# Performance work log

Hardware: AMD Instinct MI355X
Metric: run time of the kernel (lower is better)

Reference implementation:

```python
import jax, jax.numpy as jnp
import numpy as np

EPS = 1e-5

def _ln(t, g, b):
    m = t.mean(-1, keepdims=True)
    v = ((t - m) ** 2).mean(-1, keepdims=True)
    return (t - m) * jax.lax.rsqrt(v + EPS) * g + b

def _sr(t, w, b, H, W, sr):
    # t: [B, H*W, C] -> spatial-reduction conv -> [B, (H//sr)*(W//sr), C]
    B, L, C = t.shape
    xi = t.transpose(0, 2, 1).reshape(B, C, H, W)
    y = jax.lax.conv_general_dilated(xi, w, (sr, sr), 'VALID',
                                     dimension_numbers=('NCHW', 'OIHW', 'NCHW'))
    return y.reshape(B, C, -1).transpose(0, 2, 1) + b

def setup_inputs() -> dict:
    key = jax.random.key(0)
    ks = jax.random.split(key, 9)
    C, head, sr, H, W = 128, 2, 2, 64, 64
    B, N = 4, 2 * H * W
    s = 0.02
    return {
        'x': jax.random.normal(ks[0], (B, N, C), jnp.float32),
        'qW': jax.random.normal(ks[1], (C, C), jnp.float32) * s,
        'qb': jnp.zeros((C,), jnp.float32),
        'kvW': jax.random.normal(ks[2], (C, 2 * C), jnp.float32) * s,
        'kvb': jnp.zeros((2 * C,), jnp.float32),
        'projW': jax.random.normal(ks[3], (C, C), jnp.float32) * s,
        'projb': jnp.zeros((C,), jnp.float32),
        'srW': jax.random.normal(ks[4], (C, C, sr, sr), jnp.float32) * s,
        'srb': jnp.zeros((C,), jnp.float32),
        'lnW': jnp.ones((C,), jnp.float32),
        'lnB': jnp.zeros((C,), jnp.float32),
        'H': H, 'W': W, 'fuse': 1,
    }

def reference(x, qW, qb, kvW, kvb, projW, projb, srW, srb, lnW, lnB, H, W, fuse):
    head, sr = 2, 2
    B, N, C = x.shape
    Dh = C // head
    scale = Dh ** -0.5
    q = (x @ qW + qb).reshape(B, N, head, Dh).transpose(0, 2, 1, 3)  # [B,h,N,Dh]
    mask = None
    if fuse and sr > 1:
        half = N // 2
        x_rgb = _ln(_sr(x[:, :half, :], srW, srb, H, W, sr), lnW, lnB)
        x_dte = _ln(_sr(x[:, half:, :], srW, srb, H, W, sr), lnW, lnB)
        xkv = jnp.concatenate([x_rgb, x_dte], axis=1)
        M = N // (sr * sr)
        row = jnp.arange(N)[:, None] < half            # query in rgb half
        col = jnp.arange(M)[None, :] < (M // 2)        # key in rgb half
        mask = row == col                              # True on same-modality blocks -> masked
    elif sr > 1:
        xkv = _ln(_sr(x, srW, srb, H, W, sr), lnW, lnB)
    else:
        xkv = x
    M = xkv.shape[1]
    kv = (xkv @ kvW + kvb).reshape(B, M, 2, head, Dh).transpose(2, 0, 3, 1, 4)
    k, v = kv[0], kv[1]                                # [B,h,M,Dh]
    attn = jnp.einsum('bhnd,bhmd->bhnm', q, k) * scale
    if mask is not None:
        attn = jnp.where(mask[None, None], -jnp.inf, attn)
    attn = jax.nn.softmax(attn, axis=-1)
    out = jnp.einsum('bhnm,bhmd->bhnd', attn, v).transpose(0, 2, 1, 3).reshape(B, N, C)
    return out @ projW + projb
```

## Files before the change

### kernel.cpp

```cpp
#include <hip/hip_runtime.h>
#include <hip/hip_bf16.h>

#define LN_EPS 1e-5f

typedef __attribute__((ext_vector_type(8))) short bf16x8_t;
typedef __attribute__((ext_vector_type(4))) short bf16x4_t;
typedef __attribute__((ext_vector_type(4))) float f32x4_t;
typedef __attribute__((ext_vector_type(4))) unsigned short u16x4_t;

#define MFMA32(a, b, c) __builtin_amdgcn_mfma_f32_16x16x32_bf16(a, b, c, 0, 0, 0)
#define MFMA16(a, b, c) __builtin_amdgcn_mfma_f32_16x16x16bf16_1k(a, b, c, 0, 0, 0)

__device__ inline float fast_exp2(float x) {
#if __has_builtin(__builtin_amdgcn_exp2f)
    return __builtin_amdgcn_exp2f(x);
#else
    float r;
    asm volatile("v_exp_f32 %0, %1\n\ts_nop 0" : "=v"(r) : "v"(x));
    return r;
#endif
}

__device__ inline unsigned short f2bf(float f) {
    union { float f; unsigned int u; } v; v.f = f;
    unsigned int r = v.u + 0x7fffu + ((v.u >> 16) & 1u);
    return (unsigned short)(r >> 16);
}

__device__ inline u16x4_t pk4(float a, float b, float c, float d) {
    union { u16x4_t v; __hip_bfloat162 h[2]; } u;
    u.h[0] = __float22bfloat162_rn(float2{a, b});
    u.h[1] = __float22bfloat162_rn(float2{c, d});
    return u.v;
}
__device__ inline bf16x4_t pk4b(float a, float b, float c, float d) {
    union { bf16x4_t v; __hip_bfloat162 h[2]; } u;
    u.h[0] = __float22bfloat162_rn(float2{a, b});
    u.h[1] = __float22bfloat162_rn(float2{c, d});
    return u.v;
}
__device__ inline bf16x8_t pk8(float4 a, float4 b) {
    union { bf16x8_t v; __hip_bfloat162 h[4]; } u;
    u.h[0] = __float22bfloat162_rn(float2{a.x, a.y});
    u.h[1] = __float22bfloat162_rn(float2{a.z, a.w});
    u.h[2] = __float22bfloat162_rn(float2{b.x, b.y});
    u.h[3] = __float22bfloat162_rn(float2{b.z, b.w});
    return u.v;
}

__device__ inline size_t fragidx(int row, int k, int KC) {
    return ((size_t)((row >> 4) * KC + (k >> 5))) * 512 +
           (((k >> 3) & 3) * 16 + (row & 15)) * 8 + (k & 7);
}

__global__ void k_prep_w(const float* __restrict__ qW, const float* __restrict__ kvW,
                         const float* __restrict__ projW, const float* __restrict__ srW,
                         unsigned short* __restrict__ qWs, unsigned short* __restrict__ kvWs,
                         unsigned short* __restrict__ projWs, unsigned short* __restrict__ srWs) {
    int i = blockIdx.x * 256 + threadIdx.x;
    if (i < 16384) {
        int n = i & 127, k = i >> 7;
        qWs[fragidx(n, k, 4)] = f2bf(qW[k * 128 + n]);
    } else if (i < 49152) {
        int j = i - 16384; int n = j & 255, k = j >> 8;
        kvWs[fragidx(n, k, 4)] = f2bf(kvW[k * 256 + n]);
    } else if (i < 65536) {
        int j = i - 49152; int n = j & 127, k = j >> 7;
        projWs[fragidx(n, k, 4)] = f2bf(projW[k * 128 + n]);
    } else {
        int j = i - 65536; int n = j >> 9, rem = j & 511, q = rem >> 7, c = rem & 127;
        srWs[fragidx(n, q * 128 + c, 16)] = f2bf(srW[n * 512 + c * 4 + q]);
    }
}

#define XPAD 132
__global__ __launch_bounds__(256)
void k_convkv(const float* __restrict__ x, const unsigned short* __restrict__ srWs,
              const float* __restrict__ srb, const float* __restrict__ lnW,
              const float* __restrict__ lnB, const unsigned short* __restrict__ kvWs,
              const float* __restrict__ kvb, unsigned short* __restrict__ ksw,
              unsigned short* __restrict__ vls) {
    const int t = threadIdx.x, w = t >> 6, lane = t & 63;
    const int col = lane & 15, quad = lane >> 4;
    const int RT = blockIdx.x;

    __shared__ unsigned short xl[64 * XPAD];
    __shared__ unsigned short xs[4 * 512];
    __shared__ float lnred[4][16][2];

    const int pb = RT >> 7, phf = (RT >> 6) & 1;
    const int oy = (RT >> 1) & 31, ox0 = (RT & 1) * 16;
    const int n0 = phf * 4096 + 2 * oy * 64 + 2 * ox0;
    #pragma unroll
    for (int it = 0; it < 8; it++) {
        int idx = it * 256 + t;
        int chunk = idx >> 10;
        int rr = (idx >> 5) & 31;
        int c4 = idx & 31;
        float4 v = *(const float4*)(x + ((size_t)(pb * 8192 + n0 + chunk * 64 + rr)) * 128 + c4 * 4);
        *(u16x4_t*)(xl + (chunk * 32 + rr) * XPAD + c4 * 4) = pk4(v.x, v.y, v.z, v.w);
    }
    __syncthreads();

    f32x4_t acc[2] = {};
    {
        const unsigned short* wp = srWs + lane * 8;
        #pragma unroll
        for (int kc = 0; kc < 16; kc++) {
            const int q = kc >> 2, cg = kc & 3;
            const int r = (q >> 1) * 32 + 2 * col + (q & 1);
            bf16x8_t xb = *(const bf16x8_t*)(xl + r * XPAD + cg * 32 + quad * 8);
            #pragma unroll
            for (int jj = 0; jj < 2; jj++) {
                bf16x8_t wf = *(const bf16x8_t*)(wp + (size_t)((w * 2 + jj) * 16 + kc) * 512);
                acc[jj] = MFMA32(wf, xb, acc[jj]);
            }
        }
    }
    float s = 0.f, ss = 0.f;
    #pragma unroll
    for (int jj = 0; jj < 2; jj++) {
        float4 bs = *(const float4*)(srb + (w * 2 + jj) * 16 + quad * 4);
        acc[jj][0] += bs.x; acc[jj][1] += bs.y; acc[jj][2] += bs.z; acc[jj][3] += bs.w;
        #pragma unroll
        for (int r = 0; r < 4; r++) { float v = acc[jj][r]; s += v; ss += v * v; }
    }
    s += __shfl_xor(s, 16, 64);  s += __shfl_xor(s, 32, 64);
    ss += __shfl_xor(ss, 16, 64); ss += __shfl_xor(ss, 32, 64);
    if (lane < 16) { lnred[w][lane][0] = s; lnred[w][lane][1] = ss; }
    __syncthreads();
    float stot = 0.f, sstot = 0.f;
    #pragma unroll
    for (int ww = 0; ww < 4; ww++) { stot += lnred[ww][col][0]; sstot += lnred[ww][col][1]; }
    float mean = stot * (1.0f / 128.0f);
    float var = sstot * (1.0f / 128.0f) - mean * mean;
    float rs = rsqrtf(var + LN_EPS);
    #pragma unroll
    for (int jj = 0; jj < 2; jj++) {
        int f0 = (w * 2 + jj) * 16 + quad * 4;
        float4 g = *(const float4*)(lnW + f0);
        float4 be = *(const float4*)(lnB + f0);
        u16x4_t o = pk4((acc[jj][0] - mean) * rs * g.x + be.x,
                        (acc[jj][1] - mean) * rs * g.y + be.y,
                        (acc[jj][2] - mean) * rs * g.z + be.z,
                        (acc[jj][3] - mean) * rs * g.w + be.w);
        *(u16x4_t*)(xs + ((size_t)(f0 >> 5)) * 512 +
                    (((f0 >> 3) & 3) * 16 + col) * 8 + (f0 & 7)) = o;
    }
    __syncthreads();
    bf16x8_t xf[4];
    #pragma unroll
    for (int kc = 0; kc < 4; kc++)
        xf[kc] = *(const bf16x8_t*)(xs + (size_t)kc * 512 + lane * 8);
    const int p0 = RT * 16;
    const int bb = p0 >> 11;
    #pragma unroll
    for (int jj = 0; jj < 2; jj++) {
        const int nt = w * 2 + jj;
        f32x4_t aK = {};
        #pragma unroll
        for (int kc = 0; kc < 4; kc++) {
            bf16x8_t wf = *(const bf16x8_t*)(kvWs + (size_t)(nt * 4 + kc) * 512 + lane * 8);
            aK = MFMA32(wf, xf[kc], aK);
        }
        float4 bs = *(const float4*)(kvb + nt * 16 + quad * 4);
        int m = (p0 + col) & 2047;
        int bh = bb * 2 + (nt >> 2);
        int d0 = (nt & 3) * 16 + quad * 4;
        u16x4_t o = pk4(aK[0] + bs.x, aK[1] + bs.y, aK[2] + bs.z, aK[3] + bs.w);
        *(u16x4_t*)(ksw + ((size_t)(bh * 128 + (m >> 4)) * 2 + (d0 >> 5)) * 512 +
                    (((d0 >> 3) & 3) * 16 + (m & 15)) * 8 + (d0 & 7)) = o;
    }
    #pragma unroll
    for (int jj = 0; jj < 2; jj++) {
        const int nt = w * 2 + jj;
        f32x4_t aV = {};
        #pragma unroll
        for (int kc = 0; kc < 4; kc++) {
            bf16x8_t wf = *(const bf16x8_t*)(kvWs + (size_t)((8 + nt) * 4 + kc) * 512 + lane * 8);
            aV = MFMA32(xf[kc], wf, aV);
        }
        int fv = nt * 16 + col;
        int h = fv >> 6, dd = fv & 63;
        float bv = kvb[128 + fv];
        int m0 = (p0 + quad * 4) & 2047;
        int bh = bb * 2 + h;
        int kt = m0 >> 6, nb = (m0 >> 4) & 3;
        u16x4_t o = pk4(aV[0] + bv, aV[1] + bv, aV[2] + bv, aV[3] + bv);
        *(u16x4_t*)(vls + (((size_t)(bh * 32 + kt) * 4 + (dd >> 4)) * 2 + (nb >> 1)) * 512 +
                    (quad * 16 + (dd & 15)) * 8 + (nb & 1) * 4) = o;
    }
}

__global__ __launch_bounds__(256, 2)
void k_attn_f6(const float* __restrict__ x, const unsigned short* __restrict__ qWs,
               const float* __restrict__ qb, const unsigned short* __restrict__ ksw,
               const unsigned short* __restrict__ vls, const unsigned short* __restrict__ projWs,
               const float* __restrict__ projb, float* __restrict__ out) {
    const int blkx = blockIdx.x, mod = blockIdx.y, b = blockIdx.z;
    const int t = threadIdx.x, w = t >> 6, lane = t & 63;
    const int col = lane & 15, quad = lane >> 4;
    const int qg = w & 1, h = w >> 1;
    const int bh = b * 2 + h;
    const int qbase = mod * 4096 + blkx * 64 + qg * 32;

    __shared__ unsigned short sbuf[64 * 136];

    unsigned short* qarea = sbuf + w * 2048;
    const float sc = 0.125f * 1.44269504089f;
    #pragma unroll
    for (int qt = 0; qt < 2; qt++) {
        const float* xrow = x + ((size_t)b * 8192 + qbase + qt * 16 + col) * 128;
        f32x4_t acc[4] = {};
        #pragma unroll
        for (int kc = 0; kc < 4; kc++) {
            float4 xa = *(const float4*)(xrow + kc * 32 + quad * 8);
            float4 xb2 = *(const float4*)(xrow + kc * 32 + quad * 8 + 4);
            bf16x8_t xf = pk8(xa, xb2);
            #pragma unroll
            for (int j = 0; j < 4; j++) {
                bf16x8_t wf = *(const bf16x8_t*)(qWs + (size_t)((h * 4 + j) * 4 + kc) * 512 + lane * 8);
                acc[j] = MFMA32(wf, xf, acc[j]);
            }
        }
        #pragma unroll
        for (int j = 0; j < 4; j++) {
            float4 bs = *(const float4*)(qb + h * 64 + j * 16 + quad * 4);
            u16x4_t o = pk4((acc[j][0] + bs.x) * sc, (acc[j][1] + bs.y) * sc,
                            (acc[j][2] + bs.z) * sc, (acc[j][3] + bs.w) * sc);
            *(u16x4_t*)(qarea + ((size_t)(qt * 2 + (j >> 1))) * 512 +
                        (((j & 1) * 2 + (quad >> 1)) * 16 + col) * 8 + (quad & 1) * 4) = o;
        }
    }
    bf16x8_t qf[2][2];
    #pragma unroll
    for (int qt = 0; qt < 2; qt++)
        #pragma unroll
        for (int kc = 0; kc < 2; kc++)
            qf[qt][kc] = *(const bf16x8_t*)(qarea + (size_t)(qt * 2 + kc) * 512 + lane * 8);
    __syncthreads();

    const unsigned short* kp0 =
        ksw + ((size_t)(bh * 128 + (1 - mod) * 64) * 2) * 512 + lane * 8;
    const unsigned short* vp0 =
        vls + ((size_t)(bh * 32 + (1 - mod) * 16) * 8) * 512 + lane * 8;
    const bf16x4_t ones4 = { 0x3F80, 0x3F80, 0x3F80, 0x3F80 };

    f32x4_t O[2][4] = {};
    f32x4_t accl[2] = {};

    union vun { bf16x8_t v8; bf16x4_t v4[2]; };
    bf16x8_t kf0[8], kf1[8];
    vun vf0[8], vf1[8];

    auto pref0 = [&](int kt) {
        #pragma unroll
        for (int i = 0; i < 8; i++) {
            kf0[i] = *(const bf16x8_t*)(kp0 + (size_t)(kt * 8 + i) * 512);
            vf0[i].v8 = *(const bf16x8_t*)(vp0 + (size_t)(kt * 8 + i) * 512);
        }
    };
    auto pref1 = [&](int kt) {
        #pragma unroll
        for (int i = 0; i < 8; i++) {
            kf1[i] = *(const bf16x8_t*)(kp0 + (size_t)(kt * 8 + i) * 512);
            vf1[i].v8 = *(const bf16x8_t*)(vp0 + (size_t)(kt * 8 + i) * 512);
        }
    };
    auto body = [&](bf16x8_t (&kfc)[8], vun (&vfc)[8]) {
        f32x4_t ST[2][4];
        #pragma unroll
        for (int qt = 0; qt < 2; qt++)
            #pragma unroll
            for (int nb = 0; nb < 4; nb++) {
                f32x4_t sA = {};
                sA = MFMA32(kfc[nb * 2 + 0], qf[qt][0], sA);
                sA = MFMA32(kfc[nb * 2 + 1], qf[qt][1], sA);
                ST[qt][nb] = sA;
            }
        bf16x4_t pa[2][4];
        #pragma unroll
        for (int qt = 0; qt < 2; qt++)
            #pragma unroll
            for (int nb = 0; nb < 4; nb++)
                pa[qt][nb] = pk4b(fast_exp2(ST[qt][nb][0]), fast_exp2(ST[qt][nb][1]),
                                  fast_exp2(ST[qt][nb][2]), fast_exp2(ST[qt][nb][3]));
        #pragma unroll
        for (int qt = 0; qt < 2; qt++) {
            #pragma unroll
            for (int nb = 0; nb < 4; nb++) {
                accl[qt] = MFMA16(pa[qt][nb], ones4, accl[qt]);
                #pragma unroll
                for (int dt = 0; dt < 4; dt++)
                    O[qt][dt] = MFMA16(pa[qt][nb], vfc[dt * 2 + (nb >> 1)].v4[nb & 1], O[qt][dt]);
            }
        }
    };

    pref0(0);
    #pragma unroll
    for (int kt2 = 0; kt2 < 8; kt2++) {
        pref1(kt2 * 2 + 1);
        body(kf0, vf0);
        if (kt2 < 7) pref0(kt2 * 2 + 2);
        body(kf1, vf1);
    }

    #pragma unroll
    for (int qt = 0; qt < 2; qt++) {
        #pragma unroll
        for (int r = 0; r < 4; r++) {
            float rl = 1.0f / accl[qt][r];
            int qrow = qg * 32 + qt * 16 + quad * 4 + r;
            #pragma unroll
            for (int dt = 0; dt < 4; dt++)
                sbuf[qrow * 136 + h * 64 + dt * 16 + col] = f2bf(O[qt][dt][r] * rl);
        }
    }
    __syncthreads();
    {
        const int qt2 = w;
        bf16x8_t ob[4];
        #pragma unroll
        for (int kc = 0; kc < 4; kc++)
            ob[kc] = *(const bf16x8_t*)(sbuf + (size_t)(qt2 * 16 + col) * 136 + kc * 32 + quad * 8);
        f32x4_t acc[8];
        #pragma unroll
        for (int j = 0; j < 8; j++) acc[j] = f32x4_t{};
        #pragma unroll
        for (int kc = 0; kc < 4; kc++)
            #pragma unroll
            for (int j = 0; j < 8; j++) {
                bf16x8_t wf = *(const bf16x8_t*)(projWs + (size_t)(j * 4 + kc) * 512 + lane * 8);
                acc[j] = MFMA32(wf, ob[kc], acc[j]);
            }
        const int n = b * 8192 + mod * 4096 + blkx * 64 + qt2 * 16 + col;
        #pragma unroll
        for (int j = 0; j < 8; j++) {
            int f0 = j * 16 + quad * 4;
            float4 bs = *(const float4*)(projb + f0);
            float4 o = { acc[j][0] + bs.x, acc[j][1] + bs.y,
                         acc[j][2] + bs.z, acc[j][3] + bs.w };
            *(float4*)(out + (size_t)n * 128 + f0) = o;
        }
    }
}

extern "C" void kernel_launch(void* const* d_in, const int* in_sizes, int n_in,
                              void* d_out, int out_size, void* d_ws, size_t ws_size,
                              hipStream_t stream) {
    const float* x     = (const float*)d_in[0];
    const float* qW    = (const float*)d_in[1];
    const float* qb    = (const float*)d_in[2];
    const float* kvW   = (const float*)d_in[3];
    const float* kvb   = (const float*)d_in[4];
    const float* projW = (const float*)d_in[5];
    const float* projb = (const float*)d_in[6];
    const float* srW   = (const float*)d_in[7];
    const float* srb   = (const float*)d_in[8];
    const float* lnW   = (const float*)d_in[9];
    const float* lnB   = (const float*)d_in[10];

    char* ws = (char*)d_ws;
    unsigned short* qWs    = (unsigned short*)(ws + 0);
    unsigned short* kvWs   = (unsigned short*)(ws + 32768);
    unsigned short* projWs = (unsigned short*)(ws + 98304);
    unsigned short* srWs   = (unsigned short*)(ws + 131072);
    unsigned short* ksw    = (unsigned short*)(ws + 262144);
    unsigned short* vls    = (unsigned short*)(ws + 2359296);

    k_prep_w<<<dim3(512), dim3(256), 0, stream>>>(qW, kvW, projW, srW,
                                                  qWs, kvWs, projWs, srWs);
    k_convkv<<<dim3(512), dim3(256), 0, stream>>>(x, srWs, srb, lnW, lnB,
                                                  kvWs, kvb, ksw, vls);
    k_attn_f6<<<dim3(64, 2, 4), dim3(256), 0, stream>>>(x, qWs, qb, ksw, vls,
                                                        projWs, projb, (float*)d_out);
}
```

Baseline: 133.8 us.

## Use K=32 bf16 MFMA for PV by staging P through LDS and relayouting V

Switches the P·V and row-sum products from 16x16x16 MFMAs to 16x16x32 MFMAs, which halves the number of MFMA issues for that stage. The exponentiated scores are written to a per-wave LDS area and read back in the K=32 operand layout. V is stored in a matching layout by the conv/kv kernel. This adds LDS write/read traffic and an extra 16KB of shared memory per block in the inner loop, with no explicit sync inside the wave.

```diff
diff --git a/kernel.cpp b/kernel.cpp
--- a/kernel.cpp
+++ b/kernel.cpp
@@ -4,12 +4,10 @@
 #define LN_EPS 1e-5f
 
 typedef __attribute__((ext_vector_type(8))) short bf16x8_t;
-typedef __attribute__((ext_vector_type(4))) short bf16x4_t;
 typedef __attribute__((ext_vector_type(4))) float f32x4_t;
 typedef __attribute__((ext_vector_type(4))) unsigned short u16x4_t;
 
 #define MFMA32(a, b, c) __builtin_amdgcn_mfma_f32_16x16x32_bf16(a, b, c, 0, 0, 0)
-#define MFMA16(a, b, c) __builtin_amdgcn_mfma_f32_16x16x16bf16_1k(a, b, c, 0, 0, 0)
 
 __device__ inline float fast_exp2(float x) {
 #if __has_builtin(__builtin_amdgcn_exp2f)
@@ -29,12 +27,6 @@
 
 __device__ inline u16x4_t pk4(float a, float b, float c, float d) {
     union { u16x4_t v; __hip_bfloat162 h[2]; } u;
-    u.h[0] = __float22bfloat162_rn(float2{a, b});
-    u.h[1] = __float22bfloat162_rn(float2{c, d});
-    return u.v;
-}
-__device__ inline bf16x4_t pk4b(float a, float b, float c, float d) {
-    union { bf16x4_t v; __hip_bfloat162 h[2]; } u;
     u.h[0] = __float22bfloat162_rn(float2{a, b});
     u.h[1] = __float22bfloat162_rn(float2{c, d});
     return u.v;
@@ -185,15 +177,18 @@
         float bv = kvb[128 + fv];
         int m0 = (p0 + quad * 4) & 2047;
         int bh = bb * 2 + h;
-        int kt = m0 >> 6, nb = (m0 >> 4) & 3;
+        int kt = m0 >> 6;
+        int tt = (m0 >> 5) & 1;
+        int base = m0 & 31;
+        int quad_b = base >> 3, j0 = base & 7;
         u16x4_t o = pk4(aV[0] + bv, aV[1] + bv, aV[2] + bv, aV[3] + bv);
-        *(u16x4_t*)(vls + (((size_t)(bh * 32 + kt) * 4 + (dd >> 4)) * 2 + (nb >> 1)) * 512 +
-                    (quad * 16 + (dd & 15)) * 8 + (nb & 1) * 4) = o;
+        *(u16x4_t*)(vls + (((size_t)((bh * 32 + kt) * 4 + (dd >> 4)) * 2 + tt) * 512) +
+                    (quad_b * 16 + (dd & 15)) * 8 + j0) = o;
     }
 }
 
 __global__ __launch_bounds__(256, 2)
-void k_attn_f6(const float* __restrict__ x, const unsigned short* __restrict__ qWs,
+void k_attn_f7(const float* __restrict__ x, const unsigned short* __restrict__ qWs,
                const float* __restrict__ qb, const unsigned short* __restrict__ ksw,
                const unsigned short* __restrict__ vls, const unsigned short* __restrict__ projWs,
                const float* __restrict__ projb, float* __restrict__ out) {
@@ -205,6 +200,7 @@
     const int qbase = mod * 4096 + blkx * 64 + qg * 32;
 
     __shared__ unsigned short sbuf[64 * 136];
+    __shared__ unsigned short pls[4][2048];
 
     unsigned short* qarea = sbuf + w * 2048;
     const float sc = 0.125f * 1.44269504089f;
@@ -243,31 +239,31 @@
     const unsigned short* kp0 =
         ksw + ((size_t)(bh * 128 + (1 - mod) * 64) * 2) * 512 + lane * 8;
     const unsigned short* vp0 =
-        vls + ((size_t)(bh * 32 + (1 - mod) * 16) * 8) * 512 + lane * 8;
-    const bf16x4_t ones4 = { 0x3F80, 0x3F80, 0x3F80, 0x3F80 };
+        vls + ((size_t)((bh * 32 + (1 - mod) * 16) * 8)) * 512 + lane * 8;
+    const bf16x8_t ones8 = { 0x3F80, 0x3F80, 0x3F80, 0x3F80,
+                             0x3F80, 0x3F80, 0x3F80, 0x3F80 };
+    unsigned short* parea = pls[w];
 
     f32x4_t O[2][4] = {};
     f32x4_t accl[2] = {};
 
-    union vun { bf16x8_t v8; bf16x4_t v4[2]; };
-    bf16x8_t kf0[8], kf1[8];
-    vun vf0[8], vf1[8];
+    bf16x8_t kf0[8], kf1[8], vf0[8], vf1[8];
 
     auto pref0 = [&](int kt) {
         #pragma unroll
         for (int i = 0; i < 8; i++) {
             kf0[i] = *(const bf16x8_t*)(kp0 + (size_t)(kt * 8 + i) * 512);
-            vf0[i].v8 = *(const bf16x8_t*)(vp0 + (size_t)(kt * 8 + i) * 512);
+            vf0[i] = *(const bf16x8_t*)(vp0 + (size_t)(kt * 8 + i) * 512);
         }
     };
     auto pref1 = [&](int kt) {
         #pragma unroll
         for (int i = 0; i < 8; i++) {
             kf1[i] = *(const bf16x8_t*)(kp0 + (size_t)(kt * 8 + i) * 512);
-            vf1[i].v8 = *(const bf16x8_t*)(vp0 + (size_t)(kt * 8 + i) * 512);
+            vf1[i] = *(const bf16x8_t*)(vp0 + (size_t)(kt * 8 + i) * 512);
         }
     };
-    auto body = [&](bf16x8_t (&kfc)[8], vun (&vfc)[8]) {
+    auto body = [&](bf16x8_t (&kfc)[8], bf16x8_t (&vfc)[8]) {
         f32x4_t ST[2][4];
         #pragma unroll
         for (int qt = 0; qt < 2; qt++)
@@ -278,21 +274,29 @@
                 sA = MFMA32(kfc[nb * 2 + 1], qf[qt][1], sA);
                 ST[qt][nb] = sA;
             }
-        bf16x4_t pa[2][4];
         #pragma unroll
         for (int qt = 0; qt < 2; qt++)
             #pragma unroll
-            for (int nb = 0; nb < 4; nb++)
-                pa[qt][nb] = pk4b(fast_exp2(ST[qt][nb][0]), fast_exp2(ST[qt][nb][1]),
-                                  fast_exp2(ST[qt][nb][2]), fast_exp2(ST[qt][nb][3]));
+            for (int nb = 0; nb < 4; nb++) {
+                u16x4_t pk = pk4(fast_exp2(ST[qt][nb][0]), fast_exp2(ST[qt][nb][1]),
+                                 fast_exp2(ST[qt][nb][2]), fast_exp2(ST[qt][nb][3]));
+                *(u16x4_t*)(parea + qt * 1024 + (nb >> 1) * 512 +
+                            (((nb & 1) * 2 + (quad >> 1)) * 16 + col) * 8 + (quad & 1) * 4) = pk;
+            }
+        bf16x8_t pf[2][2];
         #pragma unroll
         for (int qt = 0; qt < 2; qt++) {
-            #pragma unroll
-            for (int nb = 0; nb < 4; nb++) {
-                accl[qt] = MFMA16(pa[qt][nb], ones4, accl[qt]);
-                #pragma unroll
-                for (int dt = 0; dt < 4; dt++)
-                    O[qt][dt] = MFMA16(pa[qt][nb], vfc[dt * 2 + (nb >> 1)].v4[nb & 1], O[qt][dt]);
+            pf[qt][0] = *(const bf16x8_t*)(parea + qt * 1024 + lane * 8);
+            pf[qt][1] = *(const bf16x8_t*)(parea + qt * 1024 + 512 + lane * 8);
+        }
+        #pragma unroll
+        for (int qt = 0; qt < 2; qt++) {
+            accl[qt] = MFMA32(pf[qt][0], ones8, accl[qt]);
+            accl[qt] = MFMA32(pf[qt][1], ones8, accl[qt]);
+            #pragma unroll
+            for (int dt = 0; dt < 4; dt++) {
+                O[qt][dt] = MFMA32(pf[qt][0], vfc[dt * 2 + 0], O[qt][dt]);
+                O[qt][dt] = MFMA32(pf[qt][1], vfc[dt * 2 + 1], O[qt][dt]);
             }
         }
     };
@@ -373,6 +377,6 @@
                                                   qWs, kvWs, projWs, srWs);
     k_convkv<<<dim3(512), dim3(256), 0, stream>>>(x, srWs, srb, lnW, lnB,
                                                   kvWs, kvb, ksw, vls);
-    k_attn_f6<<<dim3(64, 2, 4), dim3(256), 0, stream>>>(x, qWs, qb, ksw, vls,
+    k_attn_f7<<<dim3(64, 2, 4), dim3(256), 0, stream>>>(x, qWs, qb, ksw, vls,
                                                         projWs, projb, (float*)d_out);
 }
```

Result: no change. 132.3 us (-1.1%).
